# Kernel tuning notes

Measured on AMD Instinct MI355X. Metric: run time of the kernel, lower is better.

Reference implementation:

```python
import jax, jax.numpy as jnp
import numpy as np

N = 302       # connectome neurons
T = 2048      # R * window_size
K = 33        # inference-network temporal kernel (valid conv)
TE = T + K - 1  # extended time length before cropping
ODOR = 16
DT = 0.2


def _dwconv(x, w):
    """Per-neuron valid temporal conv. x: (N, Te), w: (N, K) -> (N, Te-K+1)."""
    return jax.lax.conv_general_dilated(
        x[None], w[:, None, :], window_strides=(1,), padding='VALID',
        feature_group_count=x.shape[0],
        dimension_numbers=('NCH', 'OIH', 'NCH'))[0]


def setup_inputs() -> dict:
    key = jax.random.key(0)
    ks = jax.random.split(key, 24)
    u = lambda k, s: jax.random.uniform(k, s, dtype=jnp.float32)
    g = lambda k, s: jax.random.normal(k, s, dtype=jnp.float32)
    inp = {}
    # forward tensor args
    inp['fluorescence_raw_target'] = u(ks[0], (N, TE))
    inp['fluorescence_full_target'] = u(ks[1], (N, T))
    inp['odor_input'] = u(ks[2], (ODOR, TE))
    inp['eps'] = g(ks[3], (N, T))  # reparameterization noise
    # encoder (Linear odor -> per-neuron sensory drive)
    inp['W_enc'] = g(ks[4], (N, ODOR)) * 0.1
    inp['b_enc'] = jnp.zeros((N,), jnp.float32)
    inp['sensory_mask'] = (u(ks[5], (N,)) < 0.15).astype(jnp.float32)
    # inference network (per-neuron depthwise temporal convs -> mu, logvar)
    inp['W_mu_f'] = g(ks[6], (N, K)) * 0.1
    inp['W_mu_s'] = g(ks[7], (N, K)) * 0.1
    inp['b_mu'] = g(ks[8], (N,)) * 0.01
    inp['W_lv_f'] = g(ks[9], (N, K)) * 0.1
    inp['W_lv_s'] = g(ks[10], (N, K)) * 0.1
    inp['b_lv'] = -2.0 + g(ks[11], (N,)) * 0.01
    # connectome-constrained recurrent weights (sparsity*signs*magnitudes folded in)
    inp['W_chem'] = (u(ks[12], (N, N)) < 0.05).astype(jnp.float32) * g(ks[13], (N, N)) * 0.1
    inp['W_elec'] = (u(ks[14], (N, N)) < 0.05).astype(jnp.float32) * g(ks[15], (N, N)) * 0.1
    inp['bias'] = g(ks[16], (N,)) * 0.1
    inp['tau'] = 0.1 + u(ks[17], (N,))
    # voltage -> calcium activation (NeuronWiseAffine)
    inp['w_aff'] = 0.5 + u(ks[18], (N,))
    inp['b_aff'] = g(ks[19], (N,)) * 0.1
    # calcium -> fluorescence (NeuronWiseLinear)
    inp['scale'] = 0.5 + u(ks[20], (N,))
    inp['shift'] = g(ks[21], (N,)) * 0.1
    # calcium decay time constant
    inp['calcium_tau'] = 0.5 + 1.5 * u(ks[22], (N,))
    return inp


def reference(fluorescence_raw_target, fluorescence_full_target, odor_input, eps,
              W_enc, b_enc, sensory_mask,
              W_mu_f, W_mu_s, b_mu, W_lv_f, W_lv_s, b_lv,
              W_chem, W_elec, bias, tau,
              w_aff, b_aff, scale, shift, calcium_tau):
    # --- encoder: sensory drive masked to sensory neurons, (N, TE) ---
    sensory_input_extend = sensory_mask[:, None] * (W_enc @ odor_input + b_enc[:, None])
    # --- inference network q(V | F, S): valid depthwise temporal convs ---
    mu_v = _dwconv(fluorescence_raw_target, W_mu_f) + _dwconv(sensory_input_extend, W_mu_s) + b_mu[:, None]
    logvar_v = _dwconv(fluorescence_raw_target, W_lv_f) + _dwconv(sensory_input_extend, W_lv_s) + b_lv[:, None]
    sample_v = mu_v + jnp.exp(0.5 * logvar_v) * eps  # (N, T)
    Tlat = mu_v.shape[1]
    crop = (sensory_input_extend.shape[1] - Tlat) // 2
    sensory_input = sensory_input_extend[:, crop:sensory_input_extend.shape[1] - crop]  # (N, T)
    # --- network dynamics: one-step leaky-integrator prediction ---
    act = jax.nn.relu(sample_v)
    recurrent_in = W_chem @ act + W_elec @ sample_v + sensory_input
    mu_neuron_voltage_prob = sample_v + (DT / tau)[:, None] * (-sample_v + recurrent_in + bias[:, None])
    # --- voltage -> calcium activation (NeuronWiseAffine, softplus) ---
    calcium_activation = jax.nn.softplus(w_aff[:, None] * sample_v + b_aff[:, None])
    # --- SCF exponential: causal exp(-t*alpha) filter + initial-calcium decay ---
    init_calcium = (fluorescence_full_target[:, 0] - shift) / scale  # (N,)
    alpha = DT / calcium_tau                               # (N,)
    t = jnp.arange(Tlat, dtype=jnp.float32)
    kern = jnp.exp(-t * alpha[:, None])                    # (N, T)
    conv = jax.vmap(lambda xn, kn: jnp.convolve(xn, kn)[:Tlat])(calcium_activation, kern)
    mu_calcium = conv + init_calcium[:, None] * kern       # (N, T)
    mu_calcium_prob = mu_calcium[None]                     # (1, N, T)
    # --- calcium -> fluorescence (NeuronWiseLinear) ---
    mu_fluorescence_trace_prob = scale[:, None] * mu_calcium + shift[:, None]
    return (mu_neuron_voltage_prob, mu_fluorescence_trace_prob, mu_v, logvar_v,
            sample_v, calcium_activation, mu_calcium_prob, recurrent_in, sensory_input)
```

## Files before the change

### kernel.cpp

```cpp
#include <hip/hip_runtime.h>
#include <hip/hip_bf16.h>

#define Nn 302
#define Tt 2048
#define TEx 2080
#define Kk 33
#define ODOR 16
#define DTc 0.2f
#define NT (Nn*Tt)
#define NMT 19

typedef __attribute__((ext_vector_type(8))) short short8;
typedef __attribute__((ext_vector_type(4))) float f32x4;

__device__ __forceinline__ unsigned short f2bu(float x){ __hip_bfloat16 h = __float2bfloat16(x); unsigned short u; __builtin_memcpy(&u, &h, 2); return u; }

__device__ __forceinline__ void ld8(const float* p, size_t i, float* v){
    float4 a = *(const float4*)(p + i);
    float4 b = *(const float4*)(p + i + 4);
    v[0]=a.x; v[1]=a.y; v[2]=a.z; v[3]=a.w;
    v[4]=b.x; v[5]=b.y; v[6]=b.z; v[7]=b.w;
}
__device__ __forceinline__ void st8(float* p, size_t i, const float* v){
    *(float4*)(p + i)     = make_float4(v[0],v[1],v[2],v[3]);
    *(float4*)(p + i + 4) = make_float4(v[4],v[5],v[6],v[7]);
}

__device__ __forceinline__ float* region(void* outv, int r){
    return (float*)outv + (size_t)r * NT;
}

__global__ __launch_bounds__(256) void kA(
    const float* __restrict__ fr, const float* __restrict__ odor,
    const float* __restrict__ eps,
    const float* __restrict__ Wenc, const float* __restrict__ benc,
    const float* __restrict__ mask,
    const float* __restrict__ Wmf, const float* __restrict__ Wms,
    const float* __restrict__ bmu,
    const float* __restrict__ Wlf, const float* __restrict__ Wls,
    const float* __restrict__ blv,
    const float* __restrict__ waff, const float* __restrict__ baff,
    const float* __restrict__ fft, const float* __restrict__ scal,
    const float* __restrict__ shft, const float* __restrict__ ctau,
    void* outv)
{
    __shared__ float frs[TEx];
    __shared__ float ses[TEx];
    __shared__ float Bsc[256];
    __shared__ float Psc[256];
    __shared__ float wv[4*Kk + ODOR];

    const int n = blockIdx.x;
    const int tid = threadIdx.x;
    float* wmf_s = wv;        float* wms_s = wv + Kk;
    float* wlf_s = wv + 2*Kk; float* wls_s = wv + 3*Kk;
    float* wenc_s = wv + 4*Kk;

    if (tid < Kk){
        wmf_s[tid] = Wmf[n*Kk+tid];
        wms_s[tid] = Wms[n*Kk+tid];
        wlf_s[tid] = Wlf[n*Kk+tid];
        wls_s[tid] = Wls[n*Kk+tid];
    }
    if (tid < ODOR) wenc_s[tid] = Wenc[n*ODOR+tid];

    for (int c = tid; c < TEx/8; c += 256){
        float v[8];
        ld8(fr, (size_t)n*TEx + c*8, v);
        #pragma unroll
        for (int j = 0; j < 8; j++) frs[c*8+j] = v[j];
    }
    __syncthreads();

    const float benc_f = benc[n];
    const float mask_f = mask[n];
    for (int c = tid; c < TEx/8; c += 256){
        float acc[8];
        #pragma unroll
        for (int j = 0; j < 8; j++) acc[j] = benc_f;
        #pragma unroll
        for (int o = 0; o < ODOR; o++){
            float v[8];
            ld8(odor, (size_t)o*TEx + c*8, v);
            #pragma unroll
            for (int j = 0; j < 8; j++) acc[j] = fmaf(wenc_s[o], v[j], acc[j]);
        }
        #pragma unroll
        for (int j = 0; j < 8; j++) ses[c*8+j] = mask_f*acc[j];
    }
    __syncthreads();

    const float bmu_f  = bmu[n];
    const float blv_f  = blv[n];
    const float waff_f = waff[n];
    const float baff_f = baff[n];

    const int t0 = tid*8;
    float xf[40], xs[40];
    #pragma unroll
    for (int i = 0; i < 10; i++){
        float4 a = *(const float4*)&frs[t0 + 4*i];
        xf[4*i]=a.x; xf[4*i+1]=a.y; xf[4*i+2]=a.z; xf[4*i+3]=a.w;
        float4 b = *(const float4*)&ses[t0 + 4*i];
        xs[4*i]=b.x; xs[4*i+1]=b.y; xs[4*i+2]=b.z; xs[4*i+3]=b.w;
    }

    float aMu[8], aLv[8];
    #pragma unroll
    for (int j = 0; j < 8; j++){ aMu[j]=bmu_f; aLv[j]=blv_f; }
    #pragma unroll
    for (int k = 0; k < Kk; k++){
        float wf=wmf_s[k], wsn=wms_s[k], vf=wlf_s[k], vsn=wls_s[k];
        #pragma unroll
        for (int j = 0; j < 8; j++){
            aMu[j] = fmaf(xf[j+k], wf, fmaf(xs[j+k], wsn, aMu[j]));
            aLv[j] = fmaf(xf[j+k], vf, fmaf(xs[j+k], vsn, aLv[j]));
        }
    }

    const size_t base = (size_t)n*Tt + t0;
    float ev[8];
    ld8(eps, base, ev);

    float smp[8], cav[8], siv[8];
    #pragma unroll
    for (int j = 0; j < 8; j++){
        float s = aMu[j] + expf(0.5f*aLv[j])*ev[j];
        smp[j] = s;
        float x = waff_f*s + baff_f;
        cav[j] = (x > 20.f) ? x : log1pf(expf(x));
        siv[j] = ses[t0 + j + 16];
    }

    st8(region(outv,2), base, aMu);
    st8(region(outv,3), base, aLv);
    st8(region(outv,4), base, smp);
    st8(region(outv,5), base, cav);
    st8(region(outv,8), base, siv);

    const float sc = scal[n];
    const float sh = shft[n];
    const float ct = ctau[n];
    const float decay = expf(-DTc/ct);

    float b = 0.f;
    #pragma unroll
    for (int j = 0; j < 8; j++) b = fmaf(decay, b, cav[j]);
    Bsc[tid] = b;
    __syncthreads();

    if (tid < 64){
        const float d2 = decay*decay, d4 = d2*d2, d8 = d4*d4;
        const float d16 = d8*d8, d32 = d16*d16;
        float g0=Bsc[4*tid], g1=Bsc[4*tid+1], g2=Bsc[4*tid+2], g3=Bsc[4*tid+3];
        float G = fmaf(d8, fmaf(d8, fmaf(d8, g0, g1), g2), g3);
        float S = G, pw = d32;
        #pragma unroll
        for (int off = 1; off < 64; off <<= 1){
            float up = __shfl_up(S, off, 64);
            if (tid >= off) S = fmaf(pw, up, S);
            pw = pw*pw;
        }
        float E = __shfl_up(S, 1, 64);
        if (tid == 0) E = 0.f;
        const float init = (fft[(size_t)n*Tt] - sh)/sc;
        float P = fmaf(init, __powf(d32, (float)tid), E);
        #pragma unroll
        for (int j = 0; j < 4; j++){ Psc[4*tid+j] = P; P = fmaf(d8, P, Bsc[4*tid+j]); }
    }
    __syncthreads();

    float c = Psc[tid];
    float mc[8], fl[8];
    #pragma unroll
    for (int j = 0; j < 8; j++){
        c = fmaf(decay, c, cav[j]);
        mc[j] = c;
        fl[j] = fmaf(sc, c, sh);
    }
    st8(region(outv,6), base, mc);
    st8(region(outv,1), base, fl);
}

__global__ __launch_bounds__(256) void kGF(
    const float* __restrict__ Wch, const float* __restrict__ Wel,
    const float* __restrict__ bias, const float* __restrict__ tau,
    void* outv)
{
    __shared__ unsigned short As[20*64*8];
    __shared__ float C[16][68];

    const int tid = threadIdx.x;
    const int wave = tid >> 6, lane = tid & 63;
    const int ln = lane & 15, quad = lane >> 4;
    const int bx = blockIdx.x, by = blockIdx.y;

    for (int s = tid; s < 20*64; s += 256){
        const int kbp = s >> 6, l = s & 63;
        const int pass = kbp / 10, kb = kbp - pass*10;
        const int lm = l & 15, lq = l >> 4;
        const int m = by*16 + lm;
        const int k0 = kb*32 + lq*8;
        const float* W = pass ? Wel : Wch;
        unsigned short v[8];
        #pragma unroll
        for (int j = 0; j < 8; j++){
            const int k = k0 + j;
            float x = (m < Nn && k < Nn) ? W[(size_t)m*Nn + k] : 0.f;
            v[j] = f2bu(x);
        }
        *(uint4*)(As + (size_t)s*8) = make_uint4(
            (unsigned)v[0]|((unsigned)v[1]<<16), (unsigned)v[2]|((unsigned)v[3]<<16),
            (unsigned)v[4]|((unsigned)v[5]<<16), (unsigned)v[6]|((unsigned)v[7]<<16));
    }
    __syncthreads();

    const float* o_sv = region(outv, 4);
    const int t = (bx*4 + wave)*16 + ln;

    f32x4 accC = {0.f,0.f,0.f,0.f};
    f32x4 accE = {0.f,0.f,0.f,0.f};
    #pragma unroll
    for (int kb = 0; kb < 10; kb++){
        const int k0 = kb*32 + quad*8;
        short8 ac = *(const short8*)(As + ((size_t)( kb     *64 + lane))*8);
        short8 ae = *(const short8*)(As + ((size_t)((10+kb)*64 + lane))*8);
        float bv[8];
        #pragma unroll
        for (int j = 0; j < 8; j++){
            int k = k0 + j;
            if (k > Nn-1) k = Nn-1;
            bv[j] = o_sv[(size_t)k*Tt + t];
        }
        short8 bc, be;
        #pragma unroll
        for (int j = 0; j < 8; j++){
            be[j] = (short)f2bu(bv[j]);
            bc[j] = (short)f2bu(fmaxf(bv[j], 0.f));
        }
        accC = __builtin_amdgcn_mfma_f32_16x16x32_bf16(ac, bc, accC, 0, 0, 0);
        accE = __builtin_amdgcn_mfma_f32_16x16x32_bf16(ae, be, accE, 0, 0, 0);
    }

    #pragma unroll
    for (int r = 0; r < 4; r++) C[quad*4 + r][wave*16 + ln] = accC[r] + accE[r];
    __syncthreads();

    if (tid < 128){
        const int m_loc = tid >> 3, strip = tid & 7;
        const int m = by*16 + m_loc;
        if (m < Nn){
            const float* o_si = region(outv, 8);
            float* o_mnv = region(outv, 0);
            float* o_rec = region(outv, 7);
            const int tt = bx*64 + strip*8;
            const size_t idx = (size_t)m*Tt + tt;
            float si[8], sv[8], rec[8], mnv[8];
            ld8(o_si, idx, si);
            ld8(o_sv, idx, sv);
            const float it = DTc / tau[m];
            const float bi = bias[m];
            #pragma unroll
            for (int j = 0; j < 8; j++){
                float rc = C[m_loc][strip*8 + j] + si[j];
                rec[j] = rc;
                mnv[j] = sv[j] + it*(-sv[j] + rc + bi);
            }
            st8(o_rec, idx, rec);
            st8(o_mnv, idx, mnv);
        }
    }
}

extern "C" void kernel_launch(void* const* d_in, const int* in_sizes, int n_in,
                              void* d_out, int out_size, void* d_ws, size_t ws_size,
                              hipStream_t stream) {
    const float* fr   = (const float*)d_in[0];
    const float* fft  = (const float*)d_in[1];
    const float* odor = (const float*)d_in[2];
    const float* eps  = (const float*)d_in[3];
    const float* Wenc = (const float*)d_in[4];
    const float* benc = (const float*)d_in[5];
    const float* mask = (const float*)d_in[6];
    const float* Wmf  = (const float*)d_in[7];
    const float* Wms  = (const float*)d_in[8];
    const float* bmu  = (const float*)d_in[9];
    const float* Wlf  = (const float*)d_in[10];
    const float* Wls  = (const float*)d_in[11];
    const float* blv  = (const float*)d_in[12];
    const float* Wch  = (const float*)d_in[13];
    const float* Wel  = (const float*)d_in[14];
    const float* bias = (const float*)d_in[15];
    const float* tau  = (const float*)d_in[16];
    const float* waff = (const float*)d_in[17];
    const float* baff = (const float*)d_in[18];
    const float* scal = (const float*)d_in[19];
    const float* shft = (const float*)d_in[20];
    const float* ctau = (const float*)d_in[21];

    (void)d_ws; (void)ws_size;

    kA<<<Nn, 256, 0, stream>>>(fr, odor, eps, Wenc, benc, mask, Wmf, Wms, bmu,
                               Wlf, Wls, blv, waff, baff, fft, scal, shft, ctau, d_out);

    kGF<<<dim3(32, NMT), 256, 0, stream>>>(Wch, Wel, bias, tau, d_out);
}
```

Baseline: 152.4 us.

## Split per-neuron kernel over time halves and move calcium scan into GEMM launch

After: 151.7 us. No clear change (-0.5%).

```diff
diff --git a/kernel.cpp b/kernel.cpp
--- a/kernel.cpp
+++ b/kernel.cpp
@@ -9,6 +9,7 @@
 #define DTc 0.2f
 #define NT (Nn*Tt)
 #define NMT 19
+#define GEMMB (32*NMT)
 
 typedef __attribute__((ext_vector_type(8))) short short8;
 typedef __attribute__((ext_vector_type(4))) float f32x4;
@@ -30,7 +31,7 @@
     return (float*)outv + (size_t)r * NT;
 }
 
-__global__ __launch_bounds__(256) void kA(
+__global__ __launch_bounds__(256) void kA1(
     const float* __restrict__ fr, const float* __restrict__ odor,
     const float* __restrict__ eps,
     const float* __restrict__ Wenc, const float* __restrict__ benc,
@@ -40,17 +41,14 @@
     const float* __restrict__ Wlf, const float* __restrict__ Wls,
     const float* __restrict__ blv,
     const float* __restrict__ waff, const float* __restrict__ baff,
-    const float* __restrict__ fft, const float* __restrict__ scal,
-    const float* __restrict__ shft, const float* __restrict__ ctau,
     void* outv)
 {
-    __shared__ float frs[TEx];
-    __shared__ float ses[TEx];
-    __shared__ float Bsc[256];
-    __shared__ float Psc[256];
+    __shared__ float frs[1056];
+    __shared__ float sess[1056];
     __shared__ float wv[4*Kk + ODOR];
 
     const int n = blockIdx.x;
+    const int c0 = blockIdx.y * 1024;
     const int tid = threadIdx.x;
     float* wmf_s = wv;        float* wms_s = wv + Kk;
     float* wlf_s = wv + 2*Kk; float* wls_s = wv + 3*Kk;
@@ -64,29 +62,18 @@
     }
     if (tid < ODOR) wenc_s[tid] = Wenc[n*ODOR+tid];
 
-    for (int c = tid; c < TEx/8; c += 256){
-        float v[8];
-        ld8(fr, (size_t)n*TEx + c*8, v);
-        #pragma unroll
-        for (int j = 0; j < 8; j++) frs[c*8+j] = v[j];
-    }
+    for (int i = tid; i < 1056; i += 256)
+        frs[i] = fr[(size_t)n*TEx + c0 + i];
     __syncthreads();
 
     const float benc_f = benc[n];
     const float mask_f = mask[n];
-    for (int c = tid; c < TEx/8; c += 256){
-        float acc[8];
-        #pragma unroll
-        for (int j = 0; j < 8; j++) acc[j] = benc_f;
-        #pragma unroll
-        for (int o = 0; o < ODOR; o++){
-            float v[8];
-            ld8(odor, (size_t)o*TEx + c*8, v);
-            #pragma unroll
-            for (int j = 0; j < 8; j++) acc[j] = fmaf(wenc_s[o], v[j], acc[j]);
-        }
-        #pragma unroll
-        for (int j = 0; j < 8; j++) ses[c*8+j] = mask_f*acc[j];
+    for (int i = tid; i < 1056; i += 256){
+        float acc = benc_f;
+        #pragma unroll
+        for (int o = 0; o < ODOR; o++)
+            acc = fmaf(wenc_s[o], odor[(size_t)o*TEx + c0 + i], acc);
+        sess[i] = mask_f*acc;
     }
     __syncthreads();
 
@@ -95,48 +82,155 @@
     const float waff_f = waff[n];
     const float baff_f = baff[n];
 
-    const int t0 = tid*8;
-    float xf[40], xs[40];
-    #pragma unroll
-    for (int i = 0; i < 10; i++){
-        float4 a = *(const float4*)&frs[t0 + 4*i];
+    const int local = tid*4;
+    float xf[37], xs[37];
+    #pragma unroll
+    for (int i = 0; i < 9; i++){
+        float4 a = *(const float4*)&frs[local + 4*i];
         xf[4*i]=a.x; xf[4*i+1]=a.y; xf[4*i+2]=a.z; xf[4*i+3]=a.w;
-        float4 b = *(const float4*)&ses[t0 + 4*i];
+        float4 b = *(const float4*)&sess[local + 4*i];
         xs[4*i]=b.x; xs[4*i+1]=b.y; xs[4*i+2]=b.z; xs[4*i+3]=b.w;
     }
-
-    float aMu[8], aLv[8];
-    #pragma unroll
-    for (int j = 0; j < 8; j++){ aMu[j]=bmu_f; aLv[j]=blv_f; }
+    xf[36] = frs[local + 36];
+    xs[36] = sess[local + 36];
+
+    float aMu[4], aLv[4];
+    #pragma unroll
+    for (int j = 0; j < 4; j++){ aMu[j]=bmu_f; aLv[j]=blv_f; }
     #pragma unroll
     for (int k = 0; k < Kk; k++){
         float wf=wmf_s[k], wsn=wms_s[k], vf=wlf_s[k], vsn=wls_s[k];
         #pragma unroll
-        for (int j = 0; j < 8; j++){
+        for (int j = 0; j < 4; j++){
             aMu[j] = fmaf(xf[j+k], wf, fmaf(xs[j+k], wsn, aMu[j]));
             aLv[j] = fmaf(xf[j+k], vf, fmaf(xs[j+k], vsn, aLv[j]));
         }
     }
 
-    const size_t base = (size_t)n*Tt + t0;
-    float ev[8];
-    ld8(eps, base, ev);
-
-    float smp[8], cav[8], siv[8];
-    #pragma unroll
-    for (int j = 0; j < 8; j++){
-        float s = aMu[j] + expf(0.5f*aLv[j])*ev[j];
+    const size_t base = (size_t)n*Tt + c0 + local;
+    float4 ev = *(const float4*)(eps + base);
+    float evv[4] = {ev.x, ev.y, ev.z, ev.w};
+
+    float smp[4], cav[4], siv[4];
+    #pragma unroll
+    for (int j = 0; j < 4; j++){
+        float s = aMu[j] + expf(0.5f*aLv[j])*evv[j];
         smp[j] = s;
         float x = waff_f*s + baff_f;
         cav[j] = (x > 20.f) ? x : log1pf(expf(x));
-        siv[j] = ses[t0 + j + 16];
-    }
-
-    st8(region(outv,2), base, aMu);
-    st8(region(outv,3), base, aLv);
-    st8(region(outv,4), base, smp);
-    st8(region(outv,5), base, cav);
-    st8(region(outv,8), base, siv);
+        siv[j] = sess[local + j + 16];
+    }
+
+    *(float4*)(region(outv,2) + base) = make_float4(aMu[0],aMu[1],aMu[2],aMu[3]);
+    *(float4*)(region(outv,3) + base) = make_float4(aLv[0],aLv[1],aLv[2],aLv[3]);
+    *(float4*)(region(outv,4) + base) = make_float4(smp[0],smp[1],smp[2],smp[3]);
+    *(float4*)(region(outv,5) + base) = make_float4(cav[0],cav[1],cav[2],cav[3]);
+    *(float4*)(region(outv,8) + base) = make_float4(siv[0],siv[1],siv[2],siv[3]);
+}
+
+__global__ __launch_bounds__(256) void kB(
+    const float* __restrict__ Wch, const float* __restrict__ Wel,
+    const float* __restrict__ bias, const float* __restrict__ tau,
+    const float* __restrict__ fft, const float* __restrict__ scal,
+    const float* __restrict__ shft, const float* __restrict__ ctau,
+    void* outv)
+{
+    __shared__ __align__(16) char smraw[20*64*8*2 + 16*68*4];
+    unsigned short* As = (unsigned short*)smraw;
+    float (*C)[68] = (float(*)[68])(smraw + 20*64*8*2);
+    float* Bsc = (float*)smraw;
+    float* Psc = (float*)(smraw + 256*4);
+
+    const int tid = threadIdx.x;
+
+    if (blockIdx.x < GEMMB){
+        const int wave = tid >> 6, lane = tid & 63;
+        const int ln = lane & 15, quad = lane >> 4;
+        const int bx = blockIdx.x & 31, by = blockIdx.x >> 5;
+
+        for (int s = tid; s < 20*64; s += 256){
+            const int kbp = s >> 6, l = s & 63;
+            const int pass = kbp / 10, kb = kbp - pass*10;
+            const int lm = l & 15, lq = l >> 4;
+            const int m = by*16 + lm;
+            const int k0 = kb*32 + lq*8;
+            const float* W = pass ? Wel : Wch;
+            unsigned short v[8];
+            #pragma unroll
+            for (int j = 0; j < 8; j++){
+                const int k = k0 + j;
+                float x = (m < Nn && k < Nn) ? W[(size_t)m*Nn + k] : 0.f;
+                v[j] = f2bu(x);
+            }
+            *(uint4*)(As + (size_t)s*8) = make_uint4(
+                (unsigned)v[0]|((unsigned)v[1]<<16), (unsigned)v[2]|((unsigned)v[3]<<16),
+                (unsigned)v[4]|((unsigned)v[5]<<16), (unsigned)v[6]|((unsigned)v[7]<<16));
+        }
+        __syncthreads();
+
+        const float* o_sv = region(outv, 4);
+        const int t = (bx*4 + wave)*16 + ln;
+
+        f32x4 accC = {0.f,0.f,0.f,0.f};
+        f32x4 accE = {0.f,0.f,0.f,0.f};
+        #pragma unroll
+        for (int kb = 0; kb < 10; kb++){
+            const int k0 = kb*32 + quad*8;
+            short8 ac = *(const short8*)(As + ((size_t)( kb     *64 + lane))*8);
+            short8 ae = *(const short8*)(As + ((size_t)((10+kb)*64 + lane))*8);
+            float bv[8];
+            #pragma unroll
+            for (int j = 0; j < 8; j++){
+                int k = k0 + j;
+                if (k > Nn-1) k = Nn-1;
+                bv[j] = o_sv[(size_t)k*Tt + t];
+            }
+            short8 bc, be;
+            #pragma unroll
+            for (int j = 0; j < 8; j++){
+                be[j] = (short)f2bu(bv[j]);
+                bc[j] = (short)f2bu(fmaxf(bv[j], 0.f));
+            }
+            accC = __builtin_amdgcn_mfma_f32_16x16x32_bf16(ac, bc, accC, 0, 0, 0);
+            accE = __builtin_amdgcn_mfma_f32_16x16x32_bf16(ae, be, accE, 0, 0, 0);
+        }
+
+        #pragma unroll
+        for (int r = 0; r < 4; r++) C[quad*4 + r][wave*16 + ln] = accC[r] + accE[r];
+        __syncthreads();
+
+        if (tid < 128){
+            const int m_loc = tid >> 3, strip = tid & 7;
+            const int m = by*16 + m_loc;
+            if (m < Nn){
+                const float* o_si = region(outv, 8);
+                float* o_mnv = region(outv, 0);
+                float* o_rec = region(outv, 7);
+                const int tt = bx*64 + strip*8;
+                const size_t idx = (size_t)m*Tt + tt;
+                float si[8], sv[8], rec[8], mnv[8];
+                ld8(o_si, idx, si);
+                ld8(o_sv, idx, sv);
+                const float it = DTc / tau[m];
+                const float bi = bias[m];
+                #pragma unroll
+                for (int j = 0; j < 8; j++){
+                    float rc = C[m_loc][strip*8 + j] + si[j];
+                    rec[j] = rc;
+                    mnv[j] = sv[j] + it*(-sv[j] + rc + bi);
+                }
+                st8(o_rec, idx, rec);
+                st8(o_mnv, idx, mnv);
+            }
+        }
+        return;
+    }
+
+    const int n = blockIdx.x - GEMMB;
+    const size_t base = (size_t)n*Tt + tid*8;
+
+    float cav[8];
+    ld8(region(outv,5), base, cav);
 
     const float sc = scal[n];
     const float sh = shft[n];
@@ -180,96 +274,6 @@
     }
     st8(region(outv,6), base, mc);
     st8(region(outv,1), base, fl);
-}
-
-__global__ __launch_bounds__(256) void kGF(
-    const float* __restrict__ Wch, const float* __restrict__ Wel,
-    const float* __restrict__ bias, const float* __restrict__ tau,
-    void* outv)
-{
-    __shared__ unsigned short As[20*64*8];
-    __shared__ float C[16][68];
-
-    const int tid = threadIdx.x;
-    const int wave = tid >> 6, lane = tid & 63;
-    const int ln = lane & 15, quad = lane >> 4;
-    const int bx = blockIdx.x, by = blockIdx.y;
-
-    for (int s = tid; s < 20*64; s += 256){
-        const int kbp = s >> 6, l = s & 63;
-        const int pass = kbp / 10, kb = kbp - pass*10;
-        const int lm = l & 15, lq = l >> 4;
-        const int m = by*16 + lm;
-        const int k0 = kb*32 + lq*8;
-        const float* W = pass ? Wel : Wch;
-        unsigned short v[8];
-        #pragma unroll
-        for (int j = 0; j < 8; j++){
-            const int k = k0 + j;
-            float x = (m < Nn && k < Nn) ? W[(size_t)m*Nn + k] : 0.f;
-            v[j] = f2bu(x);
-        }
-        *(uint4*)(As + (size_t)s*8) = make_uint4(
-            (unsigned)v[0]|((unsigned)v[1]<<16), (unsigned)v[2]|((unsigned)v[3]<<16),
-            (unsigned)v[4]|((unsigned)v[5]<<16), (unsigned)v[6]|((unsigned)v[7]<<16));
-    }
-    __syncthreads();
-
-    const float* o_sv = region(outv, 4);
-    const int t = (bx*4 + wave)*16 + ln;
-
-    f32x4 accC = {0.f,0.f,0.f,0.f};
-    f32x4 accE = {0.f,0.f,0.f,0.f};
-    #pragma unroll
-    for (int kb = 0; kb < 10; kb++){
-        const int k0 = kb*32 + quad*8;
-        short8 ac = *(const short8*)(As + ((size_t)( kb     *64 + lane))*8);
-        short8 ae = *(const short8*)(As + ((size_t)((10+kb)*64 + lane))*8);
-        float bv[8];
-        #pragma unroll
-        for (int j = 0; j < 8; j++){
-            int k = k0 + j;
-            if (k > Nn-1) k = Nn-1;
-            bv[j] = o_sv[(size_t)k*Tt + t];
-        }
-        short8 bc, be;
-        #pragma unroll
-        for (int j = 0; j < 8; j++){
-            be[j] = (short)f2bu(bv[j]);
-            bc[j] = (short)f2bu(fmaxf(bv[j], 0.f));
-        }
-        accC = __builtin_amdgcn_mfma_f32_16x16x32_bf16(ac, bc, accC, 0, 0, 0);
-        accE = __builtin_amdgcn_mfma_f32_16x16x32_bf16(ae, be, accE, 0, 0, 0);
-    }
-
-    #pragma unroll
-    for (int r = 0; r < 4; r++) C[quad*4 + r][wave*16 + ln] = accC[r] + accE[r];
-    __syncthreads();
-
-    if (tid < 128){
-        const int m_loc = tid >> 3, strip = tid & 7;
-        const int m = by*16 + m_loc;
-        if (m < Nn){
-            const float* o_si = region(outv, 8);
-            float* o_mnv = region(outv, 0);
-            float* o_rec = region(outv, 7);
-            const int tt = bx*64 + strip*8;
-            const size_t idx = (size_t)m*Tt + tt;
-            float si[8], sv[8], rec[8], mnv[8];
-            ld8(o_si, idx, si);
-            ld8(o_sv, idx, sv);
-            const float it = DTc / tau[m];
-            const float bi = bias[m];
-            #pragma unroll
-            for (int j = 0; j < 8; j++){
-                float rc = C[m_loc][strip*8 + j] + si[j];
-                rec[j] = rc;
-                mnv[j] = sv[j] + it*(-sv[j] + rc + bi);
-            }
-            st8(o_rec, idx, rec);
-            st8(o_mnv, idx, mnv);
-        }
-    }
 }
 
 extern "C" void kernel_launch(void* const* d_in, const int* in_sizes, int n_in,
@@ -300,8 +304,10 @@
 
     (void)d_ws; (void)ws_size;
 
-    kA<<<Nn, 256, 0, stream>>>(fr, odor, eps, Wenc, benc, mask, Wmf, Wms, bmu,
-                               Wlf, Wls, blv, waff, baff, fft, scal, shft, ctau, d_out);
-
-    kGF<<<dim3(32, NMT), 256, 0, stream>>>(Wch, Wel, bias, tau, d_out);
-}
+    kA1<<<dim3(Nn, 2), 256, 0, stream>>>(fr, odor, eps, Wenc, benc, mask,
+                                         Wmf, Wms, bmu, Wlf, Wls, blv,
+                                         waff, baff, d_out);
+
+    kB<<<GEMMB + Nn, 256, 0, stream>>>(Wch, Wel, bias, tau,
+                                       fft, scal, shft, ctau, d_out);
+}
```
